# Performance work log

Hardware: AMD Instinct MI355X
Metric: run time of the kernel (lower is better)

Reference implementation:

```python
import jax, jax.numpy as jnp
import numpy as np
from jax import lax

# --- configuration (matches init_kwargs) ---
NY_I = NX_I = 256      # interior model size
PML = 20               # pml width on each edge
DX = 4.0               # grid spacing (m)
DT = 5e-4              # time step (s); CFL: vmax*DT/DX ~ 0.4 < 0.5
NT = 64                # number of time steps
C1, C2 = 9.0 / 8.0, -1.0 / 24.0   # 4th-order staggered FD coefficients


def _shift(p, axis, off, n):
    idx = [slice(None)] * 3
    idx[axis] = slice(2 + off, 2 + off + n)
    return p[tuple(idx)]


def _dfwd(f, axis):
    # forward (half-cell +) staggered derivative, 4th order, zero halo
    pad = [(0, 0)] * 3
    pad[axis] = (2, 2)
    p = jnp.pad(f, pad)
    n = f.shape[axis]
    return (C1 * (_shift(p, axis, 1, n) - _shift(p, axis, 0, n))
            + C2 * (_shift(p, axis, 2, n) - _shift(p, axis, -1, n))) / DX


def _dbwd(f, axis):
    # backward (half-cell -) staggered derivative, 4th order, zero halo
    pad = [(0, 0)] * 3
    pad[axis] = (2, 2)
    p = jnp.pad(f, pad)
    n = f.shape[axis]
    return (C1 * (_shift(p, axis, 0, n) - _shift(p, axis, -1, n))
            + C2 * (_shift(p, axis, 1, n) - _shift(p, axis, -2, n))) / DX


def _propagate(lamb, mu, buoyancy, amps, src_loc, rec_loc):
    # replicate model edges into the PML region (as deepwave does)
    lambp = jnp.pad(lamb, PML, mode='edge')[None]      # [1,NY,NX]
    mup = jnp.pad(mu, PML, mode='edge')[None]
    buoyp = jnp.pad(buoyancy, PML, mode='edge')[None]
    NY, NX = lambp.shape[1], lambp.shape[2]
    n_shots = amps.shape[0]
    l2m = lambp + 2.0 * mup

    # CPML damping profiles (quadratic), alpha=0, kappa=1
    max_vel = lax.stop_gradient(jnp.max(jnp.sqrt(l2m * buoyp)))
    sig_max = 3.0 * max_vel * jnp.log(1000.0) / (2.0 * PML * DX)

    def prof(n):
        i = jnp.arange(n, dtype=lamb.dtype)
        d = jnp.maximum(jnp.clip(PML - i, 0.0, None),
                        jnp.clip(i - (n - 1 - PML), 0.0, None)) / PML
        return sig_max * d * d

    by = jnp.exp(-prof(NY) * DT)[None, :, None]
    ay = by - 1.0
    bx = jnp.exp(-prof(NX) * DT)[None, None, :]
    ax = bx - 1.0

    shot = jnp.arange(n_shots)[:, None]
    sl = src_loc + PML   # [S,nsrc,2]
    rl = rec_loc + PML   # [S,nrec,2]
    src_b = buoyp[0, sl[..., 0], sl[..., 1]]   # buoyancy at sources [S,nsrc]

    z = jnp.zeros((n_shots, NY, NX), lamb.dtype)
    carry0 = (z,) * 13  # vy,vx,syy,sxy,sxx, m_vyy,m_vyx,m_vxy,m_vxx, m_syyy,m_sxyy,m_sxyx,m_sxxx

    def step(carry, amp_t):
        (vy, vx, syy, sxy, sxx,
         mvyy, mvyx, mvxy, mvxx,
         msyyy, msxyy, msxyx, msxxx) = carry
        # --- velocity update ---
        d = _dbwd(syy, 1); msyyy = by * msyyy + ay * d; dsyy_y = d + msyyy
        d = _dbwd(sxy, 2); msxyx = bx * msxyx + ax * d; dsxy_x = d + msxyx
        vy = vy + DT * buoyp * (dsyy_y + dsxy_x)
        d = _dbwd(sxy, 1); msxyy = by * msxyy + ay * d; dsxy_y = d + msxyy
        d = _dbwd(sxx, 2); msxxx = bx * msxxx + ax * d; dsxx_x = d + msxxx
        vx = vx + DT * buoyp * (dsxy_y + dsxx_x)
        # --- inject y-oriented sources into vy ---
        vy = vy.at[shot, sl[..., 0], sl[..., 1]].add(DT * src_b * amp_t)
        # --- stress update ---
        d = _dfwd(vy, 1); mvyy = by * mvyy + ay * d; dvy_y = d + mvyy
        d = _dfwd(vx, 2); mvxx = bx * mvxx + ax * d; dvx_x = d + mvxx
        syy = syy + DT * (l2m * dvy_y + lambp * dvx_x)
        sxx = sxx + DT * (lambp * dvy_y + l2m * dvx_x)
        d = _dfwd(vy, 2); mvyx = bx * mvyx + ax * d; dvy_x = d + mvyx
        d = _dfwd(vx, 1); mvxy = by * mvxy + ay * d; dvx_y = d + mvxy
        sxy = sxy + DT * mup * (dvy_x + dvx_y)
        # --- record y-oriented receivers ---
        rec = vy[shot, rl[..., 0], rl[..., 1]]   # [S,nrec]
        return ((vy, vx, syy, sxy, sxx,
                 mvyy, mvyx, mvxy, mvxx,
                 msyyy, msxyy, msxyx, msxxx), rec)

    _, recs = lax.scan(step, carry0, jnp.moveaxis(amps, 2, 0))  # recs [nt,S,nrec]
    return jnp.transpose(recs, (1, 2, 0))  # [S,nrec,nt]


def setup_inputs() -> dict:
    key = jax.random.key(0)
    k = jax.random.split(key, 6)
    vp = 3000.0 + 100.0 * jax.random.normal(k[0], (NY_I, NX_I), jnp.float32)
    vs = 1500.0 + 50.0 * jax.random.normal(k[1], (NY_I, NX_I), jnp.float32)
    rho = 2200.0 + 50.0 * jax.random.normal(k[2], (NY_I, NX_I), jnp.float32)
    mu = rho * vs ** 2
    lamb = rho * (vp ** 2 - 2.0 * vs ** 2)
    buoyancy = 1.0 / rho
    source_amplitudes_y = jax.random.normal(k[3], (2, 8, NT), jnp.float32)
    source_locations_y = jax.random.randint(k[4], (2, 8, 2), 0, NY_I)
    receiver_locations_y = jax.random.randint(k[5], (2, 64, 2), 0, NY_I)
    return {
        'lamb': lamb, 'mu': mu, 'buoyancy': buoyancy,
        'source_amplitudes_y': source_amplitudes_y,
        'source_locations_y': source_locations_y,
        'receiver_locations_y': receiver_locations_y,
    }


def reference(lamb, mu, buoyancy, source_amplitudes_y,
              source_locations_y, receiver_locations_y):
    return _propagate(lamb, mu, buoyancy, source_amplitudes_y,
                      source_locations_y, receiver_locations_y)
```

## Files before the change

### kernel.cpp

```cpp
#include <hip/hip_runtime.h>
#include <math.h>

static constexpr int NYI  = 256;
static constexpr int PMLW = 20;
static constexpr int NY   = 296, NX = 296;
static constexpr int NCELL = NY * NX;
static constexpr int NS   = 2;
static constexpr int NSRC = 8;
static constexpr int NREC = 64;
static constexpr int NT   = 64;
static constexpr float DXF = 4.0f;
static constexpr float DTF = 5e-4f;
static constexpr float FC1 = 9.0f / 8.0f;
static constexpr float FC2 = -1.0f / 24.0f;
static constexpr float INV_DX = 1.0f / DXF;

static constexpr int TB = 8, TS = 37;
static constexpr int VS = TS + 4;
static constexpr int SS = TS + 8;
static constexpr int NBLK = TB * TB * NS;
static constexpr int NTHR = 512;
static constexpr int VAREA = VS * VS;
static constexpr int TAREA = TS * TS;
static constexpr int SFRAME = SS * SS - TAREA;
static constexpr int KV = 4, KT = 3;

static constexpr int GSLOT   = 3 * NS * NCELL;
static constexpr int FLG_OFF = 2 * GSLOT;

__device__ __forceinline__ float cohload(const float* p) {
    return __hip_atomic_load(p, __ATOMIC_RELAXED, __HIP_MEMORY_SCOPE_AGENT);
}
__device__ __forceinline__ void cohstore(float* p, float v) {
    __hip_atomic_store(p, v, __ATOMIC_RELAXED, __HIP_MEMORY_SCOPE_AGENT);
}

__global__ __launch_bounds__(NTHR, 1)
void elastic_fused(const float* __restrict__ lamb, const float* __restrict__ mu,
                   const float* __restrict__ buoy, const float* __restrict__ amps,
                   const int* __restrict__ src_loc, const int* __restrict__ rec_loc,
                   float* __restrict__ out, float* __restrict__ ws)
{
    __shared__ float sS[3][SS * SS];
    __shared__ float sV[2][VS * VS];
    __shared__ float byt[VS], ayt[VS], bxt[VS], axt[VS];
    __shared__ float sAmp[NSRC * NT];
    __shared__ float wmax[NTHR / 64];
    __shared__ int   rcnt;
    __shared__ short rl_r[NREC];
    __shared__ int   rl_pos[NREC];

    int* flags = (int*)(ws + FLG_OFF);
    float* gstr = ws;

    const int tid  = threadIdx.x;
    const int shot = blockIdx.x & 1;
    const int tb   = blockIdx.x >> 1;
    const int bty  = tb >> 3, btx = tb & 7;
    const int gy0  = bty * TS, gx0 = btx * TS;
    const int myBlk = blockIdx.x;

    int myNbr = -1;
    if (tid < 8) {
        int idx = tid < 4 ? tid : tid + 1;
        int dy = idx / 3 - 1, dx = idx % 3 - 1;
        int nty = bty + dy, ntx = btx + dx;
        if (nty >= 0 && nty < TB && ntx >= 0 && ntx < TB)
            myNbr = ((nty * TB + ntx) << 1) | shot;
    }

    for (int i = tid; i < 3 * SS * SS; i += NTHR) ((float*)sS)[i] = 0.0f;
    for (int i = tid; i < 2 * VS * VS; i += NTHR) ((float*)sV)[i] = 0.0f;
    if (tid == 0) rcnt = 0;

    float vmax = 0.0f;
    for (int i = tid * 4; i < NYI * NYI; i += NTHR * 4) {
        const float4 la4 = *(const float4*)(lamb + i);
        const float4 mu4 = *(const float4*)(mu + i);
        const float4 b4  = *(const float4*)(buoy + i);
        vmax = fmaxf(vmax, (la4.x + 2.0f * mu4.x) * b4.x);
        vmax = fmaxf(vmax, (la4.y + 2.0f * mu4.y) * b4.y);
        vmax = fmaxf(vmax, (la4.z + 2.0f * mu4.z) * b4.z);
        vmax = fmaxf(vmax, (la4.w + 2.0f * mu4.w) * b4.w);
    }
    #pragma unroll
    for (int off = 32; off > 0; off >>= 1)
        vmax = fmaxf(vmax, __shfl_down(vmax, off));
    if ((tid & 63) == 0) wmax[tid >> 6] = vmax;

    int   sidx_v[KV], vyv[KV], vxv[KV], smk[KV];
    float buo_v[KV];
    float msyyy[KV] = {0,0,0,0}, msxyx[KV] = {0,0,0,0};
    float msxyy[KV] = {0,0,0,0}, msxxx[KV] = {0,0,0,0};
    unsigned cvm = 0, intm = 0;
    #pragma unroll
    for (int k = 0; k < KV; ++k) {
        int vi = tid + NTHR * k;
        bool val = vi < VAREA;
        int vy_ = val ? vi / VS : 0;
        int vx_ = val ? vi - vy_ * VS : 0;
        int gy = gy0 - 2 + vy_, gx = gx0 - 2 + vx_;
        bool ing = val && gy >= 0 && gy < NY && gx >= 0 && gx < NX;
        if (ing) cvm |= 1u << k;
        if (ing && vy_ >= 4 && vy_ <= 37 && vx_ >= 4 && vx_ <= 37) intm |= 1u << k;
        vyv[k] = vy_; vxv[k] = vx_;
        sidx_v[k] = (vy_ + 2) * SS + (vx_ + 2);
        float b = 0.0f;
        if (ing) {
            int iy = min(max(gy - PMLW, 0), NYI - 1);
            int ix = min(max(gx - PMLW, 0), NYI - 1);
            b = buoy[iy * NYI + ix];
        }
        buo_v[k] = b;
        int sm = 0;
        #pragma unroll
        for (int s = 0; s < NSRC; ++s) {
            int sy = src_loc[(shot * NSRC + s) * 2 + 0] + PMLW;
            int sx = src_loc[(shot * NSRC + s) * 2 + 1] + PMLW;
            if (ing && sy == gy && sx == gx) sm |= 1 << s;
        }
        smk[k] = sm;
    }
    const unsigned bndm = cvm & ~intm;

    int   sidx_t[KT], vidx_t[KT], gidx_t[KT], tyt[KT], txt[KT];
    float lam_t[KT], mu_t[KT], l2m_t[KT];
    float mvyy[KT] = {0,0,0}, mvxx[KT] = {0,0,0}, mvyx[KT] = {0,0,0}, mvxy[KT] = {0,0,0};
    unsigned ctm = 0, ringm = 0;
    #pragma unroll
    for (int k = 0; k < KT; ++k) {
        int ti = tid + NTHR * k;
        bool val = ti < TAREA;
        int ty = val ? ti / TS : 0;
        int tx = val ? ti - ty * TS : 0;
        int gy = gy0 + ty, gx = gx0 + tx;
        if (val) ctm |= 1u << k;
        if (val && (ty < 4 || ty >= TS - 4 || tx < 4 || tx >= TS - 4)) ringm |= 1u << k;
        tyt[k] = ty; txt[k] = tx;
        sidx_t[k] = (ty + 4) * SS + (tx + 4);
        vidx_t[k] = (ty + 2) * VS + (tx + 2);
        gidx_t[k] = gy * NX + gx;
        float la = 0.0f, m = 0.0f;
        if (val) {
            int iy = min(max(gy - PMLW, 0), NYI - 1);
            int ix = min(max(gx - PMLW, 0), NYI - 1);
            la = lamb[iy * NYI + ix];
            m  = mu  [iy * NYI + ix];
        }
        lam_t[k] = la; mu_t[k] = m; l2m_t[k] = la + 2.0f * m;
    }

    bool fval[2], fin[2];
    int  flidx[2], fgi[2];
    #pragma unroll
    for (int k = 0; k < 2; ++k) {
        int ff = tid + NTHR * k;
        fval[k] = ff < SFRAME;
        int fy = 0, fx = 0;
        if (fval[k]) {
            if (ff < 4 * SS)      { fy = ff / SS;                 fx = ff - fy * SS; }
            else if (ff < 8 * SS) { int r = ff - 4 * SS; fy = SS - 4 + r / SS; fx = r % SS; }
            else {
                int r = ff - 8 * SS;
                if (r < (SS - 8) * 4) { fy = 4 + (r >> 2); fx = r & 3; }
                else { r -= (SS - 8) * 4; fy = 4 + (r >> 2); fx = SS - 4 + (r & 3); }
            }
        }
        int gy = gy0 - 4 + fy, gx = gx0 - 4 + fx;
        fin[k]   = fval[k] && gy >= 0 && gy < NY && gx >= 0 && gx < NX;
        flidx[k] = fy * SS + fx;
        fgi[k]   = fin[k] ? (gy * NX + gx) : 0;
    }

    __syncthreads();

    float vall = wmax[0];
    #pragma unroll
    for (int w = 1; w < NTHR / 64; ++w) vall = fmaxf(vall, wmax[w]);
    const float max_vel = sqrtf(vall);
    const float sig_max = 3.0f * max_vel * logf(1000.0f) / (2.0f * PMLW * DXF);
    if (tid < VS) {
        auto prof = [&](int g) -> float {
            float fi = (float)g;
            float d1 = fmaxf((float)PMLW - fi, 0.0f);
            float d2 = fmaxf(fi - (float)(NY - 1 - PMLW), 0.0f);
            float dd = fmaxf(d1, d2) * (1.0f / (float)PMLW);
            return expf(-(sig_max * dd * dd) * DTF);
        };
        float b = prof(gy0 - 2 + tid); byt[tid] = b; ayt[tid] = b - 1.0f;
        b = prof(gx0 - 2 + tid);       bxt[tid] = b; axt[tid] = b - 1.0f;
    }
    if (tid < NREC) {
        int r = tid;
        int ry = rec_loc[(shot * NREC + r) * 2 + 0] + PMLW;
        int rx = rec_loc[(shot * NREC + r) * 2 + 1] + PMLW;
        if (ry >= gy0 && ry < gy0 + TS && rx >= gx0 && rx < gx0 + TS) {
            int p = atomicAdd(&rcnt, 1);
            rl_r[p]   = (short)r;
            rl_pos[p] = (ry - gy0 + 2) * VS + (rx - gx0 + 2);
        }
    }
    for (int i = tid; i < NSRC * NT; i += NTHR)
        sAmp[i] = amps[shot * NSRC * NT + i];
    __syncthreads();

    auto do_vel = [&](unsigned m, int t) {
        #pragma unroll
        for (int k = 0; k < KV; ++k) {
            if (!((m >> k) & 1)) continue;
            int si = sidx_v[k];
            float by_ = byt[vyv[k]], ay_ = ayt[vyv[k]];
            float bx_ = bxt[vxv[k]], ax_ = axt[vxv[k]];
            float d, mm;
            d = (FC1 * (sS[0][si] - sS[0][si - SS]) + FC2 * (sS[0][si + SS] - sS[0][si - 2 * SS])) * INV_DX;
            mm = by_ * msyyy[k] + ay_ * d;  msyyy[k] = mm;  float dsyy_y = d + mm;
            d = (FC1 * (sS[1][si] - sS[1][si - 1]) + FC2 * (sS[1][si + 1] - sS[1][si - 2])) * INV_DX;
            mm = bx_ * msxyx[k] + ax_ * d;  msxyx[k] = mm;  float dsxy_x = d + mm;
            d = (FC1 * (sS[1][si] - sS[1][si - SS]) + FC2 * (sS[1][si + SS] - sS[1][si - 2 * SS])) * INV_DX;
            mm = by_ * msxyy[k] + ay_ * d;  msxyy[k] = mm;  float dsxy_y = d + mm;
            d = (FC1 * (sS[2][si] - sS[2][si - 1]) + FC2 * (sS[2][si + 1] - sS[2][si - 2])) * INV_DX;
            mm = bx_ * msxxx[k] + ax_ * d;  msxxx[k] = mm;  float dsxx_x = d + mm;
            int vi = tid + NTHR * k;
            float nvy = sV[0][vi] + DTF * buo_v[k] * (dsyy_y + dsxy_x);
            float nvx = sV[1][vi] + DTF * buo_v[k] * (dsxy_y + dsxx_x);
            if (smk[k]) {
                #pragma unroll
                for (int s = 0; s < NSRC; ++s)
                    if ((smk[k] >> s) & 1) nvy += DTF * buo_v[k] * sAmp[s * NT + t];
            }
            sV[0][vi] = nvy;
            sV[1][vi] = nvx;
        }
    };

    for (int t = 0; t < NT; ++t) {
        const float* gsr = gstr + ((t + 1) & 1) * GSLOT;
        float*       gsw = gstr + (t & 1) * GSLOT;

        do_vel(intm, t);

        if (t > 0 && myNbr >= 0) {
            while (__hip_atomic_load(&flags[myNbr], __ATOMIC_RELAXED,
                                     __HIP_MEMORY_SCOPE_AGENT) < t)
                __builtin_amdgcn_s_sleep(1);
        }
        __syncthreads();

        float fr0[3], fr1[3];
        #pragma unroll
        for (int f = 0; f < 3; ++f) {
            fr0[f] = (t > 0 && fin[0]) ? cohload(&gsr[(f * NS + shot) * NCELL + fgi[0]]) : 0.0f;
            fr1[f] = (t > 0 && fin[1]) ? cohload(&gsr[(f * NS + shot) * NCELL + fgi[1]]) : 0.0f;
        }
        if (fval[0]) { sS[0][flidx[0]] = fr0[0]; sS[1][flidx[0]] = fr0[1]; sS[2][flidx[0]] = fr0[2]; }
        if (fval[1]) { sS[0][flidx[1]] = fr1[0]; sS[1][flidx[1]] = fr1[1]; sS[2][flidx[1]] = fr1[2]; }
        __syncthreads();

        do_vel(bndm, t);
        __syncthreads();

        if (tid < rcnt)
            out[(shot * NREC + rl_r[tid]) * NT + t] = sV[0][rl_pos[tid]];

        #pragma unroll
        for (int k = 0; k < KT; ++k) {
            if (!((ctm >> k) & 1)) continue;
            int si = sidx_t[k], vi = vidx_t[k];
            float by_ = byt[tyt[k] + 2], ay_ = ayt[tyt[k] + 2];
            float bx_ = bxt[txt[k] + 2], ax_ = axt[txt[k] + 2];
            float d, mm;
            d = (FC1 * (sV[0][vi + VS] - sV[0][vi]) + FC2 * (sV[0][vi + 2 * VS] - sV[0][vi - VS])) * INV_DX;
            mm = by_ * mvyy[k] + ay_ * d;  mvyy[k] = mm;  float dvy_y = d + mm;
            d = (FC1 * (sV[1][vi + 1] - sV[1][vi]) + FC2 * (sV[1][vi + 2] - sV[1][vi - 1])) * INV_DX;
            mm = bx_ * mvxx[k] + ax_ * d;  mvxx[k] = mm;  float dvx_x = d + mm;
            float nsyy = sS[0][si] + DTF * (l2m_t[k] * dvy_y + lam_t[k] * dvx_x);
            float nsxx = sS[2][si] + DTF * (lam_t[k] * dvy_y + l2m_t[k] * dvx_x);
            d = (FC1 * (sV[0][vi + 1] - sV[0][vi]) + FC2 * (sV[0][vi + 2] - sV[0][vi - 1])) * INV_DX;
            mm = bx_ * mvyx[k] + ax_ * d;  mvyx[k] = mm;  float dvy_x = d + mm;
            d = (FC1 * (sV[1][vi + VS] - sV[1][vi]) + FC2 * (sV[1][vi + 2 * VS] - sV[1][vi - VS])) * INV_DX;
            mm = by_ * mvxy[k] + ay_ * d;  mvxy[k] = mm;  float dvx_y = d + mm;
            float nsxy = sS[1][si] + DTF * mu_t[k] * (dvy_x + dvx_y);
            sS[0][si] = nsyy; sS[1][si] = nsxy; sS[2][si] = nsxx;
            if ((ringm >> k) & 1) {
                int gi = gidx_t[k];
                cohstore(&gsw[(0 * NS + shot) * NCELL + gi], nsyy);
                cohstore(&gsw[(1 * NS + shot) * NCELL + gi], nsxy);
                cohstore(&gsw[(2 * NS + shot) * NCELL + gi], nsxx);
            }
        }

        __syncthreads();
        if (tid == 0 && t < NT - 1)
            __hip_atomic_store(&flags[myBlk], t + 1, __ATOMIC_RELAXED,
                               __HIP_MEMORY_SCOPE_AGENT);
    }
}

extern "C" void kernel_launch(void* const* d_in, const int* in_sizes, int n_in,
                              void* d_out, int out_size, void* d_ws, size_t ws_size,
                              hipStream_t stream) {
    const float* lamb    = (const float*)d_in[0];
    const float* mu      = (const float*)d_in[1];
    const float* buoy    = (const float*)d_in[2];
    const float* amps    = (const float*)d_in[3];
    const int*   src_loc = (const int*)d_in[4];
    const int*   rec_loc = (const int*)d_in[5];
    float* ws  = (float*)d_ws;
    float* out = (float*)d_out;

    hipMemsetAsync(ws + FLG_OFF, 0, NBLK * sizeof(int), stream);

    elastic_fused<<<NBLK, NTHR, 0, stream>>>(lamb, mu, buoy, amps, src_loc, rec_loc, out, ws);
}
```

Baseline: 340.0 us.

## Widen halos to exchange neighbor data every two time steps instead of one

Halos in shared memory grow to 6 cells for stress and 4 for velocity. Each block now computes redundant boundary cells so it can advance two time steps between inter-block flag exchanges, which halves the number of global spin-wait synchronisations. In exchange, each exchange publishes and reloads many more fields, including velocities and the CPML memory variables. The redundant halo computation also adds arithmetic and shared-memory traffic per step.

```diff
diff --git a/kernel.cpp b/kernel.cpp
--- a/kernel.cpp
+++ b/kernel.cpp
@@ -16,16 +16,22 @@
 static constexpr float INV_DX = 1.0f / DXF;
 
 static constexpr int TB = 8, TS = 37;
-static constexpr int VS = TS + 4;
-static constexpr int SS = TS + 8;
 static constexpr int NBLK = TB * TB * NS;
 static constexpr int NTHR = 512;
-static constexpr int VAREA = VS * VS;
-static constexpr int TAREA = TS * TS;
-static constexpr int SFRAME = SS * SS - TAREA;
-static constexpr int KV = 4, KT = 3;
-
-static constexpr int GSLOT   = 3 * NS * NCELL;
+
+static constexpr int SS2 = TS + 12;
+static constexpr int VS2 = TS + 9;
+static constexpr int SAREA = SS2 * SS2;
+static constexpr int VAREA = VS2 * VS2;
+static constexpr int S1W = TS + 6;
+static constexpr int S1AREA = S1W * S1W;
+static constexpr int KV = 5, KS = 4;
+static constexpr int SFRAME = SAREA - TS * TS;
+static constexpr int VFRAME = VAREA - 40 * 40;
+static constexpr int NROUND = NT / 2;
+
+static constexpr int NFLD = 13;
+static constexpr int GSLOT   = NFLD * NS * NCELL;
 static constexpr int FLG_OFF = 2 * GSLOT;
 
 __device__ __forceinline__ float cohload(const float* p) {
@@ -41,9 +47,9 @@
                    const int* __restrict__ src_loc, const int* __restrict__ rec_loc,
                    float* __restrict__ out, float* __restrict__ ws)
 {
-    __shared__ float sS[3][SS * SS];
-    __shared__ float sV[2][VS * VS];
-    __shared__ float byt[VS], ayt[VS], bxt[VS], axt[VS];
+    __shared__ float sS[3][SAREA];
+    __shared__ float sV[2][VAREA];
+    __shared__ float byt[SS2], ayt[SS2], bxt[SS2], axt[SS2];
     __shared__ float sAmp[NSRC * NT];
     __shared__ float wmax[NTHR / 64];
     __shared__ int   rcnt;
@@ -69,8 +75,8 @@
             myNbr = ((nty * TB + ntx) << 1) | shot;
     }
 
-    for (int i = tid; i < 3 * SS * SS; i += NTHR) ((float*)sS)[i] = 0.0f;
-    for (int i = tid; i < 2 * VS * VS; i += NTHR) ((float*)sV)[i] = 0.0f;
+    for (int i = tid; i < 3 * SAREA; i += NTHR) ((float*)sS)[i] = 0.0f;
+    for (int i = tid; i < 2 * VAREA; i += NTHR) ((float*)sV)[i] = 0.0f;
     if (tid == 0) rcnt = 0;
 
     float vmax = 0.0f;
@@ -88,23 +94,27 @@
         vmax = fmaxf(vmax, __shfl_down(vmax, off));
     if ((tid & 63) == 0) wmax[tid >> 6] = vmax;
 
-    int   sidx_v[KV], vyv[KV], vxv[KV], smk[KV];
+    int   vpk[KV], smk[KV];
     float buo_v[KV];
-    float msyyy[KV] = {0,0,0,0}, msxyx[KV] = {0,0,0,0};
-    float msxyy[KV] = {0,0,0,0}, msxxx[KV] = {0,0,0,0};
-    unsigned cvm = 0, intm = 0;
+    float ms0[KV] = {0,0,0,0,0}, ms1[KV] = {0,0,0,0,0};
+    float ms2[KV] = {0,0,0,0,0}, ms3[KV] = {0,0,0,0,0};
+    unsigned mA = 0, mAint = 0, mB = 0, mVring = 0, mMsfr = 0;
     #pragma unroll
     for (int k = 0; k < KV; ++k) {
         int vi = tid + NTHR * k;
         bool val = vi < VAREA;
-        int vy_ = val ? vi / VS : 0;
-        int vx_ = val ? vi - vy_ * VS : 0;
-        int gy = gy0 - 2 + vy_, gx = gx0 - 2 + vx_;
+        int vyl = val ? vi / VS2 : 0;
+        int vxl = val ? vi - vyl * VS2 : 0;
+        int gy = gy0 + vyl - 4, gx = gx0 + vxl - 4;
         bool ing = val && gy >= 0 && gy < NY && gx >= 0 && gx < NX;
-        if (ing) cvm |= 1u << k;
-        if (ing && vy_ >= 4 && vy_ <= 37 && vx_ >= 4 && vx_ <= 37) intm |= 1u << k;
-        vyv[k] = vy_; vxv[k] = vx_;
-        sidx_v[k] = (vy_ + 2) * SS + (vx_ + 2);
+        if (ing) mA |= 1u << k;
+        if (ing && vyl >= 6 && vyl <= 39 && vxl >= 6 && vxl <= 39) mAint |= 1u << k;
+        if (ing && vyl >= 3 && vyl <= 42 && vxl >= 3 && vxl <= 42) mB |= 1u << k;
+        int cy = vyl - 4, cx = vxl - 4;
+        bool tile = cy >= 0 && cy <= 36 && cx >= 0 && cx <= 36;
+        if (val && tile && (cy < 6 || cy >= 31 || cx < 6 || cx >= 31)) mVring |= 1u << k;
+        if (ing && (vyl < 3 || vyl > 42 || vxl < 3 || vxl > 42)) mMsfr |= 1u << k;
+        vpk[k] = (vyl << 8) | vxl;
         float b = 0.0f;
         if (ing) {
             int iy = min(max(gy - PMLW, 0), NYI - 1);
@@ -121,27 +131,30 @@
         }
         smk[k] = sm;
     }
-    const unsigned bndm = cvm & ~intm;
-
-    int   sidx_t[KT], vidx_t[KT], gidx_t[KT], tyt[KT], txt[KT];
-    float lam_t[KT], mu_t[KT], l2m_t[KT];
-    float mvyy[KT] = {0,0,0}, mvxx[KT] = {0,0,0}, mvyx[KT] = {0,0,0}, mvxy[KT] = {0,0,0};
-    unsigned ctm = 0, ringm = 0;
-    #pragma unroll
-    for (int k = 0; k < KT; ++k) {
-        int ti = tid + NTHR * k;
-        bool val = ti < TAREA;
-        int ty = val ? ti / TS : 0;
-        int tx = val ? ti - ty * TS : 0;
-        int gy = gy0 + ty, gx = gx0 + tx;
-        if (val) ctm |= 1u << k;
-        if (val && (ty < 4 || ty >= TS - 4 || tx < 4 || tx >= TS - 4)) ringm |= 1u << k;
-        tyt[k] = ty; txt[k] = tx;
-        sidx_t[k] = (ty + 4) * SS + (tx + 4);
-        vidx_t[k] = (ty + 2) * VS + (tx + 2);
-        gidx_t[k] = gy * NX + gx;
+
+    int   spk[KS], gvi_s[KS];
+    float lam_t[KS], mu_t[KS], l2m_t[KS];
+    float mv0[KS] = {0,0,0,0}, mv1[KS] = {0,0,0,0};
+    float mv2[KS] = {0,0,0,0}, mv3[KS] = {0,0,0,0};
+    unsigned mS1 = 0, mS2 = 0, mSring = 0, mMvfr = 0;
+    #pragma unroll
+    for (int k = 0; k < KS; ++k) {
+        int si = tid + NTHR * k;
+        bool val = si < S1AREA;
+        int sy = val ? si / S1W : 0;
+        int sx = val ? si - sy * S1W : 0;
+        int gy = gy0 + sy - 3, gx = gx0 + sx - 3;
+        bool ing = val && gy >= 0 && gy < NY && gx >= 0 && gx < NX;
+        if (ing) mS1 |= 1u << k;
+        int cy = sy - 3, cx = sx - 3;
+        bool tile = cy >= 0 && cy <= 36 && cx >= 0 && cx <= 36;
+        if (val && tile) mS2 |= 1u << k;
+        if (val && tile && (cy < 6 || cy >= 31 || cx < 6 || cx >= 31)) mSring |= 1u << k;
+        if (ing && !tile) mMvfr |= 1u << k;
+        spk[k] = (sy << 8) | sx;
+        gvi_s[k] = ing ? gy * NX + gx : 0;
         float la = 0.0f, m = 0.0f;
-        if (val) {
+        if (ing) {
             int iy = min(max(gy - PMLW, 0), NYI - 1);
             int ix = min(max(gx - PMLW, 0), NYI - 1);
             la = lamb[iy * NYI + ix];
@@ -150,26 +163,37 @@
         lam_t[k] = la; mu_t[k] = m; l2m_t[k] = la + 2.0f * m;
     }
 
-    bool fval[2], fin[2];
-    int  flidx[2], fgi[2];
+    bool sfin[3]; int sfl[3], sfg[3];
+    #pragma unroll
+    for (int k = 0; k < 3; ++k) {
+        int ff = tid + NTHR * k;
+        bool fv = ff < SFRAME;
+        int fy = 0, fx = 0;
+        if (fv) {
+            if (ff < 6 * SS2)        { fy = ff / SS2; fx = ff - fy * SS2; }
+            else if (ff < 12 * SS2)  { int r2 = ff - 6 * SS2; fy = 43 + r2 / SS2; fx = r2 % SS2; }
+            else { int r2 = ff - 12 * SS2; fy = 6 + r2 / 12; int c = r2 % 12; fx = c < 6 ? c : 37 + c; }
+        }
+        int gy = gy0 + fy - 6, gx = gx0 + fx - 6;
+        sfin[k] = fv && gy >= 0 && gy < NY && gx >= 0 && gx < NX;
+        sfl[k] = fy * SS2 + fx;
+        sfg[k] = sfin[k] ? gy * NX + gx : 0;
+    }
+    bool vfin[2]; int vfl[2], vfg[2];
     #pragma unroll
     for (int k = 0; k < 2; ++k) {
         int ff = tid + NTHR * k;
-        fval[k] = ff < SFRAME;
+        bool fv = ff < VFRAME;
         int fy = 0, fx = 0;
-        if (fval[k]) {
-            if (ff < 4 * SS)      { fy = ff / SS;                 fx = ff - fy * SS; }
-            else if (ff < 8 * SS) { int r = ff - 4 * SS; fy = SS - 4 + r / SS; fx = r % SS; }
-            else {
-                int r = ff - 8 * SS;
-                if (r < (SS - 8) * 4) { fy = 4 + (r >> 2); fx = r & 3; }
-                else { r -= (SS - 8) * 4; fy = 4 + (r >> 2); fx = SS - 4 + (r & 3); }
-            }
-        }
-        int gy = gy0 - 4 + fy, gx = gx0 - 4 + fx;
-        fin[k]   = fval[k] && gy >= 0 && gy < NY && gx >= 0 && gx < NX;
-        flidx[k] = fy * SS + fx;
-        fgi[k]   = fin[k] ? (gy * NX + gx) : 0;
+        if (fv) {
+            if (ff < 3 * VS2)        { fy = ff / VS2; fx = ff - fy * VS2; }
+            else if (ff < 6 * VS2)   { int r2 = ff - 3 * VS2; fy = 43 + r2 / VS2; fx = r2 % VS2; }
+            else { int r2 = ff - 6 * VS2; fy = 3 + r2 / 6; int c = r2 % 6; fx = c < 3 ? c : 40 + c; }
+        }
+        int gy = gy0 + fy - 4, gx = gx0 + fx - 4;
+        vfin[k] = fv && gy >= 0 && gy < NY && gx >= 0 && gx < NX;
+        vfl[k] = fy * VS2 + fx;
+        vfg[k] = vfin[k] ? gy * NX + gx : 0;
     }
 
     __syncthreads();
@@ -179,7 +203,7 @@
     for (int w = 1; w < NTHR / 64; ++w) vall = fmaxf(vall, wmax[w]);
     const float max_vel = sqrtf(vall);
     const float sig_max = 3.0f * max_vel * logf(1000.0f) / (2.0f * PMLW * DXF);
-    if (tid < VS) {
+    if (tid < SS2) {
         auto prof = [&](int g) -> float {
             float fi = (float)g;
             float d1 = fmaxf((float)PMLW - fi, 0.0f);
@@ -187,8 +211,8 @@
             float dd = fmaxf(d1, d2) * (1.0f / (float)PMLW);
             return expf(-(sig_max * dd * dd) * DTF);
         };
-        float b = prof(gy0 - 2 + tid); byt[tid] = b; ayt[tid] = b - 1.0f;
-        b = prof(gx0 - 2 + tid);       bxt[tid] = b; axt[tid] = b - 1.0f;
+        float b = prof(gy0 - 6 + tid); byt[tid] = b; ayt[tid] = b - 1.0f;
+        b = prof(gx0 - 6 + tid);       bxt[tid] = b; axt[tid] = b - 1.0f;
     }
     if (tid < NREC) {
         int r = tid;
@@ -197,30 +221,31 @@
         if (ry >= gy0 && ry < gy0 + TS && rx >= gx0 && rx < gx0 + TS) {
             int p = atomicAdd(&rcnt, 1);
             rl_r[p]   = (short)r;
-            rl_pos[p] = (ry - gy0 + 2) * VS + (rx - gx0 + 2);
+            rl_pos[p] = (ry - gy0 + 4) * VS2 + (rx - gx0 + 4);
         }
     }
     for (int i = tid; i < NSRC * NT; i += NTHR)
         sAmp[i] = amps[shot * NSRC * NT + i];
     __syncthreads();
 
-    auto do_vel = [&](unsigned m, int t) {
+    auto do_vel = [&](unsigned m, int t, bool pub, float* gsw) {
         #pragma unroll
         for (int k = 0; k < KV; ++k) {
             if (!((m >> k) & 1)) continue;
-            int si = sidx_v[k];
-            float by_ = byt[vyv[k]], ay_ = ayt[vyv[k]];
-            float bx_ = bxt[vxv[k]], ax_ = axt[vxv[k]];
+            const int vi = tid + NTHR * k;
+            const int vyl = vpk[k] >> 8, vxl = vpk[k] & 255;
+            const int si = (vyl + 2) * SS2 + (vxl + 2);
+            const float by_ = byt[vyl + 2], ay_ = ayt[vyl + 2];
+            const float bx_ = bxt[vxl + 2], ax_ = axt[vxl + 2];
             float d, mm;
-            d = (FC1 * (sS[0][si] - sS[0][si - SS]) + FC2 * (sS[0][si + SS] - sS[0][si - 2 * SS])) * INV_DX;
-            mm = by_ * msyyy[k] + ay_ * d;  msyyy[k] = mm;  float dsyy_y = d + mm;
+            d = (FC1 * (sS[0][si] - sS[0][si - SS2]) + FC2 * (sS[0][si + SS2] - sS[0][si - 2 * SS2])) * INV_DX;
+            mm = by_ * ms0[k] + ay_ * d;  ms0[k] = mm;  const float dsyy_y = d + mm;
             d = (FC1 * (sS[1][si] - sS[1][si - 1]) + FC2 * (sS[1][si + 1] - sS[1][si - 2])) * INV_DX;
-            mm = bx_ * msxyx[k] + ax_ * d;  msxyx[k] = mm;  float dsxy_x = d + mm;
-            d = (FC1 * (sS[1][si] - sS[1][si - SS]) + FC2 * (sS[1][si + SS] - sS[1][si - 2 * SS])) * INV_DX;
-            mm = by_ * msxyy[k] + ay_ * d;  msxyy[k] = mm;  float dsxy_y = d + mm;
+            mm = bx_ * ms1[k] + ax_ * d;  ms1[k] = mm;  const float dsxy_x = d + mm;
+            d = (FC1 * (sS[1][si] - sS[1][si - SS2]) + FC2 * (sS[1][si + SS2] - sS[1][si - 2 * SS2])) * INV_DX;
+            mm = by_ * ms2[k] + ay_ * d;  ms2[k] = mm;  const float dsxy_y = d + mm;
             d = (FC1 * (sS[2][si] - sS[2][si - 1]) + FC2 * (sS[2][si + 1] - sS[2][si - 2])) * INV_DX;
-            mm = bx_ * msxxx[k] + ax_ * d;  msxxx[k] = mm;  float dsxx_x = d + mm;
-            int vi = tid + NTHR * k;
+            mm = bx_ * ms3[k] + ax_ * d;  ms3[k] = mm;  const float dsxx_x = d + mm;
             float nvy = sV[0][vi] + DTF * buo_v[k] * (dsyy_y + dsxy_x);
             float nvx = sV[1][vi] + DTF * buo_v[k] * (dsxy_y + dsxx_x);
             if (smk[k]) {
@@ -230,68 +255,128 @@
             }
             sV[0][vi] = nvy;
             sV[1][vi] = nvx;
+            if (pub && ((mVring >> k) & 1)) {
+                const int gvi = (gy0 + vyl - 4) * NX + (gx0 + vxl - 4);
+                cohstore(&gsw[(3 * NS + shot) * NCELL + gvi], nvy);
+                cohstore(&gsw[(4 * NS + shot) * NCELL + gvi], nvx);
+                cohstore(&gsw[(5 * NS + shot) * NCELL + gvi], ms0[k]);
+                cohstore(&gsw[(6 * NS + shot) * NCELL + gvi], ms1[k]);
+                cohstore(&gsw[(7 * NS + shot) * NCELL + gvi], ms2[k]);
+                cohstore(&gsw[(8 * NS + shot) * NCELL + gvi], ms3[k]);
+            }
         }
     };
 
-    for (int t = 0; t < NT; ++t) {
-        const float* gsr = gstr + ((t + 1) & 1) * GSLOT;
-        float*       gsw = gstr + (t & 1) * GSLOT;
-
-        do_vel(intm, t);
-
-        if (t > 0 && myNbr >= 0) {
+    auto do_stress = [&](unsigned m, bool pub, float* gsw) {
+        #pragma unroll
+        for (int k = 0; k < KS; ++k) {
+            if (!((m >> k) & 1)) continue;
+            const int sy = spk[k] >> 8, sx = spk[k] & 255;
+            const int si = (sy + 3) * SS2 + (sx + 3);
+            const int vi = (sy + 1) * VS2 + (sx + 1);
+            const float by_ = byt[sy + 3], ay_ = ayt[sy + 3];
+            const float bx_ = bxt[sx + 3], ax_ = axt[sx + 3];
+            float d, mm;
+            d = (FC1 * (sV[0][vi + VS2] - sV[0][vi]) + FC2 * (sV[0][vi + 2 * VS2] - sV[0][vi - VS2])) * INV_DX;
+            mm = by_ * mv0[k] + ay_ * d;  mv0[k] = mm;  const float dvy_y = d + mm;
+            d = (FC1 * (sV[1][vi + 1] - sV[1][vi]) + FC2 * (sV[1][vi + 2] - sV[1][vi - 1])) * INV_DX;
+            mm = bx_ * mv1[k] + ax_ * d;  mv1[k] = mm;  const float dvx_x = d + mm;
+            const float nsyy = sS[0][si] + DTF * (l2m_t[k] * dvy_y + lam_t[k] * dvx_x);
+            const float nsxx = sS[2][si] + DTF * (lam_t[k] * dvy_y + l2m_t[k] * dvx_x);
+            d = (FC1 * (sV[0][vi + 1] - sV[0][vi]) + FC2 * (sV[0][vi + 2] - sV[0][vi - 1])) * INV_DX;
+            mm = bx_ * mv2[k] + ax_ * d;  mv2[k] = mm;  const float dvy_x = d + mm;
+            d = (FC1 * (sV[1][vi + VS2] - sV[1][vi]) + FC2 * (sV[1][vi + 2 * VS2] - sV[1][vi - VS2])) * INV_DX;
+            mm = by_ * mv3[k] + ay_ * d;  mv3[k] = mm;  const float dvx_y = d + mm;
+            const float nsxy = sS[1][si] + DTF * mu_t[k] * (dvy_x + dvx_y);
+            sS[0][si] = nsyy; sS[1][si] = nsxy; sS[2][si] = nsxx;
+            if (pub && ((mSring >> k) & 1)) {
+                const int gvi = gvi_s[k];
+                cohstore(&gsw[(0 * NS + shot) * NCELL + gvi], nsyy);
+                cohstore(&gsw[(1 * NS + shot) * NCELL + gvi], nsxy);
+                cohstore(&gsw[(2 * NS + shot) * NCELL + gvi], nsxx);
+                cohstore(&gsw[(9  * NS + shot) * NCELL + gvi], mv0[k]);
+                cohstore(&gsw[(10 * NS + shot) * NCELL + gvi], mv1[k]);
+                cohstore(&gsw[(11 * NS + shot) * NCELL + gvi], mv2[k]);
+                cohstore(&gsw[(12 * NS + shot) * NCELL + gvi], mv3[k]);
+            }
+        }
+    };
+
+    for (int r = 0; r < NROUND; ++r) {
+        const float* gsr = gstr + ((r + 1) & 1) * GSLOT;
+        float*       gsw = gstr + (r & 1) * GSLOT;
+        const int t0 = 2 * r;
+        const bool pubr = (r < NROUND - 1);
+
+        do_vel(mAint, t0, false, gsw);
+
+        if (r > 0 && myNbr >= 0) {
             while (__hip_atomic_load(&flags[myNbr], __ATOMIC_RELAXED,
-                                     __HIP_MEMORY_SCOPE_AGENT) < t)
+                                     __HIP_MEMORY_SCOPE_AGENT) < r)
                 __builtin_amdgcn_s_sleep(1);
         }
         __syncthreads();
 
-        float fr0[3], fr1[3];
-        #pragma unroll
-        for (int f = 0; f < 3; ++f) {
-            fr0[f] = (t > 0 && fin[0]) ? cohload(&gsr[(f * NS + shot) * NCELL + fgi[0]]) : 0.0f;
-            fr1[f] = (t > 0 && fin[1]) ? cohload(&gsr[(f * NS + shot) * NCELL + fgi[1]]) : 0.0f;
-        }
-        if (fval[0]) { sS[0][flidx[0]] = fr0[0]; sS[1][flidx[0]] = fr0[1]; sS[2][flidx[0]] = fr0[2]; }
-        if (fval[1]) { sS[0][flidx[1]] = fr1[0]; sS[1][flidx[1]] = fr1[1]; sS[2][flidx[1]] = fr1[2]; }
-        __syncthreads();
-
-        do_vel(bndm, t);
+        if (r > 0) {
+            float a0[3][3], b0[2][2];
+            #pragma unroll
+            for (int k = 0; k < 3; ++k)
+                #pragma unroll
+                for (int f = 0; f < 3; ++f)
+                    a0[k][f] = sfin[k] ? cohload(&gsr[(f * NS + shot) * NCELL + sfg[k]]) : 0.0f;
+            #pragma unroll
+            for (int k = 0; k < 2; ++k)
+                #pragma unroll
+                for (int f = 0; f < 2; ++f)
+                    b0[k][f] = vfin[k] ? cohload(&gsr[((3 + f) * NS + shot) * NCELL + vfg[k]]) : 0.0f;
+            #pragma unroll
+            for (int k = 0; k < KV; ++k) {
+                if ((mMsfr >> k) & 1) {
+                    const int vyl = vpk[k] >> 8, vxl = vpk[k] & 255;
+                    const int gvi = (gy0 + vyl - 4) * NX + (gx0 + vxl - 4);
+                    ms0[k] = cohload(&gsr[(5 * NS + shot) * NCELL + gvi]);
+                    ms1[k] = cohload(&gsr[(6 * NS + shot) * NCELL + gvi]);
+                    ms2[k] = cohload(&gsr[(7 * NS + shot) * NCELL + gvi]);
+                    ms3[k] = cohload(&gsr[(8 * NS + shot) * NCELL + gvi]);
+                }
+            }
+            #pragma unroll
+            for (int k = 0; k < KS; ++k) {
+                if ((mMvfr >> k) & 1) {
+                    const int gvi = gvi_s[k];
+                    mv0[k] = cohload(&gsr[(9  * NS + shot) * NCELL + gvi]);
+                    mv1[k] = cohload(&gsr[(10 * NS + shot) * NCELL + gvi]);
+                    mv2[k] = cohload(&gsr[(11 * NS + shot) * NCELL + gvi]);
+                    mv3[k] = cohload(&gsr[(12 * NS + shot) * NCELL + gvi]);
+                }
+            }
+            #pragma unroll
+            for (int k = 0; k < 3; ++k)
+                if (sfin[k]) { sS[0][sfl[k]] = a0[k][0]; sS[1][sfl[k]] = a0[k][1]; sS[2][sfl[k]] = a0[k][2]; }
+            #pragma unroll
+            for (int k = 0; k < 2; ++k)
+                if (vfin[k]) { sV[0][vfl[k]] = b0[k][0]; sV[1][vfl[k]] = b0[k][1]; }
+        }
+        __syncthreads();
+
+        do_vel(mA & ~mAint, t0, false, gsw);
         __syncthreads();
 
         if (tid < rcnt)
-            out[(shot * NREC + rl_r[tid]) * NT + t] = sV[0][rl_pos[tid]];
-
-        #pragma unroll
-        for (int k = 0; k < KT; ++k) {
-            if (!((ctm >> k) & 1)) continue;
-            int si = sidx_t[k], vi = vidx_t[k];
-            float by_ = byt[tyt[k] + 2], ay_ = ayt[tyt[k] + 2];
-            float bx_ = bxt[txt[k] + 2], ax_ = axt[txt[k] + 2];
-            float d, mm;
-            d = (FC1 * (sV[0][vi + VS] - sV[0][vi]) + FC2 * (sV[0][vi + 2 * VS] - sV[0][vi - VS])) * INV_DX;
-            mm = by_ * mvyy[k] + ay_ * d;  mvyy[k] = mm;  float dvy_y = d + mm;
-            d = (FC1 * (sV[1][vi + 1] - sV[1][vi]) + FC2 * (sV[1][vi + 2] - sV[1][vi - 1])) * INV_DX;
-            mm = bx_ * mvxx[k] + ax_ * d;  mvxx[k] = mm;  float dvx_x = d + mm;
-            float nsyy = sS[0][si] + DTF * (l2m_t[k] * dvy_y + lam_t[k] * dvx_x);
-            float nsxx = sS[2][si] + DTF * (lam_t[k] * dvy_y + l2m_t[k] * dvx_x);
-            d = (FC1 * (sV[0][vi + 1] - sV[0][vi]) + FC2 * (sV[0][vi + 2] - sV[0][vi - 1])) * INV_DX;
-            mm = bx_ * mvyx[k] + ax_ * d;  mvyx[k] = mm;  float dvy_x = d + mm;
-            d = (FC1 * (sV[1][vi + VS] - sV[1][vi]) + FC2 * (sV[1][vi + 2 * VS] - sV[1][vi - VS])) * INV_DX;
-            mm = by_ * mvxy[k] + ay_ * d;  mvxy[k] = mm;  float dvx_y = d + mm;
-            float nsxy = sS[1][si] + DTF * mu_t[k] * (dvy_x + dvx_y);
-            sS[0][si] = nsyy; sS[1][si] = nsxy; sS[2][si] = nsxx;
-            if ((ringm >> k) & 1) {
-                int gi = gidx_t[k];
-                cohstore(&gsw[(0 * NS + shot) * NCELL + gi], nsyy);
-                cohstore(&gsw[(1 * NS + shot) * NCELL + gi], nsxy);
-                cohstore(&gsw[(2 * NS + shot) * NCELL + gi], nsxx);
-            }
-        }
-
-        __syncthreads();
-        if (tid == 0 && t < NT - 1)
-            __hip_atomic_store(&flags[myBlk], t + 1, __ATOMIC_RELAXED,
+            out[(shot * NREC + rl_r[tid]) * NT + t0] = sV[0][rl_pos[tid]];
+        do_stress(mS1, false, gsw);
+        __syncthreads();
+
+        do_vel(mB, t0 + 1, pubr, gsw);
+        __syncthreads();
+
+        if (tid < rcnt)
+            out[(shot * NREC + rl_r[tid]) * NT + t0 + 1] = sV[0][rl_pos[tid]];
+        do_stress(mS2, pubr, gsw);
+
+        __syncthreads();
+        if (tid == 0 && r < NROUND - 1)
+            __hip_atomic_store(&flags[myBlk], r + 1, __ATOMIC_RELAXED,
                                __HIP_MEMORY_SCOPE_AGENT);
     }
 }
```

New measurement: 1.079 ms. 217% more time.

## Split velocity-max reduction across blocks with atomic grid-wide combine

Applied to the files above, without the earlier changes.

Previously every block scanned the whole 256x256 lamb, mu and buoyancy arrays to find the maximum velocity for the PML profile, so the full model was read once per block. Now each block reduces a disjoint 512-element slice. The per-block maxima are combined with a global atomic max on the float bit pattern, which is valid because the values are positive, and a spin-wait counter barrier makes all blocks wait for the result. This removes the redundant global reads but adds a grid-wide barrier, which relies on every block being co-resident and on two extra workspace words being zeroed before launch.

```diff
diff --git a/kernel.cpp b/kernel.cpp
--- a/kernel.cpp
+++ b/kernel.cpp
@@ -73,20 +73,14 @@
     for (int i = tid; i < 2 * VS * VS; i += NTHR) ((float*)sV)[i] = 0.0f;
     if (tid == 0) rcnt = 0;
 
-    float vmax = 0.0f;
-    for (int i = tid * 4; i < NYI * NYI; i += NTHR * 4) {
-        const float4 la4 = *(const float4*)(lamb + i);
-        const float4 mu4 = *(const float4*)(mu + i);
-        const float4 b4  = *(const float4*)(buoy + i);
-        vmax = fmaxf(vmax, (la4.x + 2.0f * mu4.x) * b4.x);
-        vmax = fmaxf(vmax, (la4.y + 2.0f * mu4.y) * b4.y);
-        vmax = fmaxf(vmax, (la4.z + 2.0f * mu4.z) * b4.z);
-        vmax = fmaxf(vmax, (la4.w + 2.0f * mu4.w) * b4.w);
-    }
-    #pragma unroll
-    for (int off = 32; off > 0; off >>= 1)
-        vmax = fmaxf(vmax, __shfl_down(vmax, off));
-    if ((tid & 63) == 0) wmax[tid >> 6] = vmax;
+    {
+        int i = myBlk * NTHR + tid;
+        float v = (lamb[i] + 2.0f * mu[i]) * buoy[i];
+        #pragma unroll
+        for (int off = 32; off > 0; off >>= 1)
+            v = fmaxf(v, __shfl_down(v, off));
+        if ((tid & 63) == 0) wmax[tid >> 6] = v;
+    }
 
     int   sidx_v[KV], vyv[KV], vxv[KV], smk[KV];
     float buo_v[KV];
@@ -174,10 +168,23 @@
 
     __syncthreads();
 
-    float vall = wmax[0];
-    #pragma unroll
-    for (int w = 1; w < NTHR / 64; ++w) vall = fmaxf(vall, wmax[w]);
-    const float max_vel = sqrtf(vall);
+    if (tid == 0) {
+        float v = wmax[0];
+        #pragma unroll
+        for (int w = 1; w < NTHR / 64; ++w) v = fmaxf(v, wmax[w]);
+        unsigned* gmx = (unsigned*)(flags + NBLK);
+        int*      gcnt = flags + NBLK + 1;
+        __hip_atomic_fetch_max(gmx, __float_as_uint(v), __ATOMIC_RELAXED,
+                               __HIP_MEMORY_SCOPE_AGENT);
+        __hip_atomic_fetch_add(gcnt, 1, __ATOMIC_RELEASE, __HIP_MEMORY_SCOPE_AGENT);
+        while (__hip_atomic_load(gcnt, __ATOMIC_ACQUIRE, __HIP_MEMORY_SCOPE_AGENT) < NBLK)
+            __builtin_amdgcn_s_sleep(1);
+        unsigned mb = __hip_atomic_load(gmx, __ATOMIC_RELAXED, __HIP_MEMORY_SCOPE_AGENT);
+        wmax[0] = __uint_as_float(mb);
+    }
+    __syncthreads();
+
+    const float max_vel = sqrtf(wmax[0]);
     const float sig_max = 3.0f * max_vel * logf(1000.0f) / (2.0f * PMLW * DXF);
     if (tid < VS) {
         auto prof = [&](int g) -> float {
@@ -308,7 +315,7 @@
     float* ws  = (float*)d_ws;
     float* out = (float*)d_out;
 
-    hipMemsetAsync(ws + FLG_OFF, 0, NBLK * sizeof(int), stream);
+    hipMemsetAsync(ws + FLG_OFF, 0, (NBLK + 2) * sizeof(int), stream);
 
     elastic_fused<<<NBLK, NTHR, 0, stream>>>(lamb, mu, buoy, amps, src_loc, rec_loc, out, ws);
 }
```

Measured after the change: 350.7 us. +3.1%, slower.
